# Optimization experiments

Measured on AMD Instinct MI355X. Metric: run time of the kernel, lower is better.

Reference implementation:

```python
import jax, jax.numpy as jnp
import numpy as np

N, E, G = 10000, 160000, 64      # nodes, edges, graphs
IN, H, L = 128, 128, 14          # in_channels, hidden, num GENConv layers
EPS_LN = 1e-5                    # torch LayerNorm eps
EPS_MSG = 1e-7                   # GENConv message eps


def layer_norm(x, g, b):
    mu = jnp.mean(x, axis=-1, keepdims=True)
    v = jnp.var(x, axis=-1, keepdims=True)
    return (x - mu) * jax.lax.rsqrt(v + EPS_LN) * g + b


def gen_conv(h, src, dst, t, sc, W1, b1, mg, mb, W2, b2):
    # message: relu(x_j) + eps  (no edge_attr)
    msg = jax.nn.relu(h[src]) + EPS_MSG                      # [E, H]
    # softmax aggregation over edges sharing a destination, per feature
    z = msg * t
    mx = jax.ops.segment_max(z, dst, num_segments=N)         # [N, H]
    mx = jnp.where(jnp.isfinite(mx), mx, 0.0)
    e = jnp.exp(z - mx[dst])
    ssum = jax.ops.segment_sum(e, dst, num_segments=N)
    alpha = e / (ssum[dst] + 1e-16)
    agg = jax.ops.segment_sum(msg * alpha, dst, num_segments=N)  # [N, H]
    # MessageNorm: normalize(agg) * ||h|| * scale
    agg = agg / jnp.maximum(jnp.linalg.norm(agg, axis=-1, keepdims=True), 1e-12)
    agg = agg * jnp.linalg.norm(h, axis=-1, keepdims=True) * sc
    out = h + agg
    # MLP [H, 2H, H] with LayerNorm + ReLU between (dropout off in eval)
    z1 = layer_norm(out @ W1 + b1, mg, mb)
    return jax.nn.relu(z1) @ W2 + b2


def setup_inputs() -> dict:
    key = jax.random.key(0)
    ks = jax.random.split(key, 8)
    s = 0.05
    x = jax.random.normal(ks[0], (N, IN), jnp.float32)
    edge_index = jax.random.randint(ks[1], (2, E), 0, N, dtype=jnp.int64)
    batch = jnp.sort(jax.random.randint(ks[2], (N,), 0, G, dtype=jnp.int64))
    enc_W = jax.random.normal(ks[3], (IN, H), jnp.float32) * s
    enc_b = jnp.zeros((H,), jnp.float32)
    ln_g = jnp.ones((L, H), jnp.float32)
    ln_b = jnp.zeros((L, H), jnp.float32)
    t = jnp.ones((L,), jnp.float32)         # learnable softmax temperature
    scale = jnp.ones((L,), jnp.float32)     # learnable MsgNorm scale
    W1 = jax.random.normal(ks[4], (L, H, 2 * H), jnp.float32) * s
    b1 = jnp.zeros((L, 2 * H), jnp.float32)
    mg = jnp.ones((L, 2 * H), jnp.float32)
    mb = jnp.zeros((L, 2 * H), jnp.float32)
    W2 = jax.random.normal(ks[5], (L, 2 * H, H), jnp.float32) * s
    b2 = jnp.zeros((L, H), jnp.float32)
    fn_g = jnp.ones((H,), jnp.float32)
    fn_b = jnp.zeros((H,), jnp.float32)
    return dict(x=x, edge_index=edge_index, batch=batch, enc_W=enc_W, enc_b=enc_b,
                ln_g=ln_g, ln_b=ln_b, t=t, scale=scale, W1=W1, b1=b1, mg=mg, mb=mb,
                W2=W2, b2=b2, fn_g=fn_g, fn_b=fn_b)


def reference(x, edge_index, batch, enc_W, enc_b, ln_g, ln_b, t, scale,
              W1, b1, mg, mb, W2, b2, fn_g, fn_b):
    src, dst = edge_index[0], edge_index[1]
    h = x @ enc_W + enc_b
    for i in range(L):  # DeepGCNLayer 'res+': x + conv(act(norm(x)))
        r = jax.nn.leaky_relu(layer_norm(h, ln_g[i], ln_b[i]), 0.01)
        h = h + gen_conv(r, src, dst, t[i], scale[i],
                         W1[i], b1[i], mg[i], mb[i], W2[i], b2[i])
    h = jax.nn.leaky_relu(layer_norm(h, fn_g, fn_b), 0.01)
    # global_mean_pool (fin_map is unused in the original forward)
    cnt = jax.ops.segment_sum(jnp.ones((N,), h.dtype), batch, num_segments=G)
    gf = jax.ops.segment_sum(h, batch, num_segments=G) / jnp.maximum(cnt, 1.0)[:, None]
    return gf
```

## Files before the change

### kernel.cpp

```cpp
#include <hip/hip_runtime.h>
#include <cstdint>
#include <cstddef>


#define BT 512

typedef __attribute__((ext_vector_type(8))) short bf16x8;
typedef __attribute__((ext_vector_type(4))) float f32x4;

__device__ inline float bf2f(ushort u) {
    union { uint i; float f; } v;
    v.i = (uint)u << 16;
    return v.f;
}
__device__ inline ushort f2bf(float f) {
    union { float f; uint i; } v;
    v.f = f;
    return (ushort)((v.i + 0x7fffu + ((v.i >> 16) & 1u)) >> 16);
}
__device__ inline uint f2bf2(float a, float b) {
    return (uint)f2bf(a) | ((uint)f2bf(b) << 16);
}

__device__ inline float wave_sum_f(float v) {
#pragma unroll
    for (int off = 32; off > 0; off >>= 1) v += __shfl_xor(v, off, 64);
    return v;
}

__global__ void setup_kernel(const float* __restrict__ x, ushort* __restrict__ xb,
                             const int* __restrict__ dst, int* __restrict__ deg,
                             const int* __restrict__ batch, int* __restrict__ gstart,
                             int total, int N, int E, int G) {
    int idx = blockIdx.x * blockDim.x + threadIdx.x;
    if (idx >= total) return;
    xb[idx] = f2bf(x[idx]);
    if (idx < E) atomicAdd(&deg[dst[idx]], 1);
    if (idx < N) {
        int bb = batch[idx];
        if (idx == 0)
            for (int g = 0; g <= bb; g++) gstart[g] = 0;
        else {
            int pb = batch[idx - 1];
            for (int g = pb + 1; g <= bb; g++) gstart[g] = idx;
        }
        if (idx == N - 1)
            for (int g = bb + 1; g <= G; g++) gstart[g] = N;
    }
}

__global__ __launch_bounds__(1024) void scan_kernel(const int* __restrict__ deg,
                                                    int* __restrict__ offs,
                                                    int* __restrict__ cursor, int N) {
    __shared__ int part[1024];
    int tid = threadIdx.x;
    int CH = (N + 1023) / 1024;
    int base = tid * CH;
    int s = 0;
    for (int i = 0; i < CH; i++) {
        int idx = base + i;
        if (idx < N) s += deg[idx];
    }
    part[tid] = s;
    __syncthreads();
    for (int off = 1; off < 1024; off <<= 1) {
        int v = (tid >= off) ? part[tid - off] : 0;
        __syncthreads();
        part[tid] += v;
        __syncthreads();
    }
    int run = (tid == 0) ? 0 : part[tid - 1];
    for (int i = 0; i < CH; i++) {
        int idx = base + i;
        if (idx < N) {
            offs[idx] = run;
            cursor[idx] = run;
            run += deg[idx];
        }
    }
    if (tid == 1023) offs[N] = part[1023];
}

__global__ void scatter_kernel(const int* __restrict__ src, const int* __restrict__ dst,
                               int* __restrict__ cursor, int* __restrict__ esrc, int E) {
    int e = blockIdx.x * blockDim.x + threadIdx.x;
    if (e < E) {
        int d = dst[e];
        int pos = atomicAdd(&cursor[d], 1);
        esrc[pos] = src[e];
    }
}

__global__ __launch_bounds__(256) void prep_kernel(const float* __restrict__ W1,
                                                   const float* __restrict__ W2,
                                                   const float* __restrict__ encW,
                                                   ushort* __restrict__ W1t,
                                                   ushort* __restrict__ W2t,
                                                   ushort* __restrict__ encWt, int L) {
    __shared__ float tile[32][33];
    int z = blockIdx.z;
    const float* in;
    ushort* out;
    int R, C;
    if (z < L) {
        in = W1 + (size_t)z * 32768; out = W1t + (size_t)z * 32768; R = 128; C = 256;
    } else if (z < 2 * L) {
        int i = z - L;
        in = W2 + (size_t)i * 32768; out = W2t + (size_t)i * 32768; R = 256; C = 128;
    } else {
        in = encW; out = encWt; R = 128; C = 128;
    }
    int r0 = blockIdx.y * 32, c0 = blockIdx.x * 32;
    if (r0 >= R || c0 >= C) return;
    int tx = threadIdx.x & 31, ty = threadIdx.x >> 5;
    for (int i = ty; i < 32; i += 8) tile[i][tx] = in[(size_t)(r0 + i) * C + c0 + tx];
    __syncthreads();
    for (int i = ty; i < 32; i += 8)
        out[(size_t)(c0 + i) * R + r0 + tx] = f2bf(tile[tx][i]);
}

__device__ __forceinline__ void agg_stage_v9(const ushort* __restrict__ rin,
                                             const int* __restrict__ offs,
                                             const int* __restrict__ esrc,
                                             const float* __restrict__ rnbuf,
                                             float tv, float sv, int row0,
                                             int w, int l, uint (*AsU)[68]) {
    int nd0 = row0 + 2 * w;
    int a0 = offs[nd0], a1 = offs[nd0 + 1], a2 = offs[nd0 + 2];
    int eb[2] = {a0, a1};
    int dg[2] = {a1 - a0, a2 - a1};
    float cs[2][4][2] = {}, cw[2][4][2] = {};
    int mx = max((dg[0] + 3) >> 2, (dg[1] + 3) >> 2);
#pragma unroll 1
    for (int i = 0; i < mx; i++) {
        int j = i * 4;
        uint rv[2][4];
        bool vl[2][4];
#pragma unroll
        for (int k = 0; k < 2; k++)
#pragma unroll
            for (int c = 0; c < 4; c++) {
                int jj = j + c;
                vl[k][c] = jj < dg[k];
                if (vl[k][c]) {
                    int sn = esrc[eb[k] + jj];
                    rv[k][c] = ((const uint*)rin)[(size_t)sn * 64 + l];
                }
            }
#pragma unroll
        for (int k = 0; k < 2; k++)
#pragma unroll
            for (int c = 0; c < 4; c++) {
                if (vl[k][c]) {
                    float x0 = bf2f((ushort)(rv[k][c] & 0xffff));
                    float x1 = bf2f((ushort)(rv[k][c] >> 16));
                    float g0 = fmaxf(x0, 0.f) + 1e-7f;
                    float g1 = fmaxf(x1, 0.f) + 1e-7f;
                    float p0 = __expf(g0 * tv);
                    float p1 = __expf(g1 * tv);
                    cs[k][c][0] += p0;
                    cs[k][c][1] += p1;
                    cw[k][c][0] += g0 * p0;
                    cw[k][c][1] += g1 * p1;
                }
            }
    }
#pragma unroll
    for (int k = 0; k < 2; k++) {
        float s0 = (cs[k][0][0] + cs[k][1][0]) + (cs[k][2][0] + cs[k][3][0]);
        float s1 = (cs[k][0][1] + cs[k][1][1]) + (cs[k][2][1] + cs[k][3][1]);
        float W0 = (cw[k][0][0] + cw[k][1][0]) + (cw[k][2][0] + cw[k][3][0]);
        float W1 = (cw[k][0][1] + cw[k][1][1]) + (cw[k][2][1] + cw[k][3][1]);
        float agg0 = W0 / (s0 + 1e-16f);
        float agg1 = W1 / (s1 + 1e-16f);
        int nd = nd0 + k;
        float nr = sqrtf(wave_sum_f(agg0 * agg0 + agg1 * agg1));
        float fac = rnbuf[nd] * sv / fmaxf(nr, 1e-12f);
        uint ru = ((const uint*)rin)[(size_t)nd * 64 + l];
        AsU[2 * w + k][l] = f2bf2(bf2f((ushort)(ru & 0xffff)) + agg0 * fac,
                                  bf2f((ushort)(ru >> 16)) + agg1 * fac);
    }
}

__device__ __forceinline__ void gemm1_stage8(const ushort (*As)[136],
                                             const ushort* __restrict__ Bt,
                                             const float* __restrict__ bias,
                                             const float* __restrict__ mg,
                                             const float* __restrict__ mb,
                                             ushort (*z1s)[264],
                                             int w, int q, int ln,
                                             float (*pS)[16], float (*pQ)[16]) {
    f32x4 acc[2];
    acc[0] = (f32x4){0.f, 0.f, 0.f, 0.f};
    acc[1] = (f32x4){0.f, 0.f, 0.f, 0.f};
#pragma unroll
    for (int ks = 0; ks < 128; ks += 32) {
        bf16x8 a = *(const bf16x8*)&As[ln][ks + q * 8];
#pragma unroll
        for (int ct = 0; ct < 2; ct++) {
            bf16x8 bv = *(const bf16x8*)(Bt + (size_t)(w * 32 + ct * 16 + ln) * 128 + ks + q * 8);
            acc[ct] = __builtin_amdgcn_mfma_f32_16x16x32_bf16(a, bv, acc[ct], 0, 0, 0);
        }
    }
    float s1[4] = {0, 0, 0, 0}, s2[4] = {0, 0, 0, 0};
#pragma unroll
    for (int ct = 0; ct < 2; ct++)
#pragma unroll
        for (int r = 0; r < 4; r++) {
            float v = acc[ct][r] + bias[w * 32 + ct * 16 + ln];
            acc[ct][r] = v;
            s1[r] += v;
            s2[r] += v * v;
        }
#pragma unroll
    for (int off = 1; off < 16; off <<= 1)
#pragma unroll
        for (int r = 0; r < 4; r++) {
            s1[r] += __shfl_xor(s1[r], off, 64);
            s2[r] += __shfl_xor(s2[r], off, 64);
        }
    if (ln == 0)
#pragma unroll
        for (int r = 0; r < 4; r++) {
            pS[w][q * 4 + r] = s1[r];
            pQ[w][q * 4 + r] = s2[r];
        }
    __syncthreads();
#pragma unroll
    for (int r = 0; r < 4; r++) {
        int row = q * 4 + r;
        float S = 0.f, Q = 0.f;
#pragma unroll
        for (int ww = 0; ww < 8; ww++) {
            S += pS[ww][row];
            Q += pQ[ww][row];
        }
        float mu = S * (1.f / 256.f);
        float var = Q * (1.f / 256.f) - mu * mu;
        float rs = rsqrtf(var + 1e-5f);
#pragma unroll
        for (int ct = 0; ct < 2; ct++) {
            int col = w * 32 + ct * 16 + ln;
            float y = (acc[ct][r] - mu) * rs * mg[col] + mb[col];
            z1s[row][col] = f2bf(fmaxf(y, 0.f));
        }
    }
    __syncthreads();
}

template <int KD, bool RESID>
__device__ __forceinline__ void out_stage8(const ushort* __restrict__ Abase, int astr,
                                           const ushort* __restrict__ Bt,
                                           const float* __restrict__ bias,
                                           const float* __restrict__ lg,
                                           const float* __restrict__ lb,
                                           float* __restrict__ hbuf,
                                           ushort* __restrict__ rout,
                                           float* __restrict__ rnbuf,
                                           int row0, int w, int q, int ln,
                                           float (*pS)[16], float (*pQ)[16]) {
    f32x4 acc = (f32x4){0.f, 0.f, 0.f, 0.f};
    int col = w * 16 + ln;
#pragma unroll
    for (int ks = 0; ks < KD; ks += 32) {
        bf16x8 a = *(const bf16x8*)(Abase + ln * astr + ks + q * 8);
        bf16x8 bv = *(const bf16x8*)(Bt + (size_t)col * KD + ks + q * 8);
        acc = __builtin_amdgcn_mfma_f32_16x16x32_bf16(a, bv, acc, 0, 0, 0);
    }
    float s1[4], s2[4];
#pragma unroll
    for (int r = 0; r < 4; r++) {
        int row = q * 4 + r;
        float v = acc[r] + bias[col];
        if (RESID) v += hbuf[(size_t)(row0 + row) * 128 + col];
        hbuf[(size_t)(row0 + row) * 128 + col] = v;
        acc[r] = v;
        s1[r] = v;
        s2[r] = v * v;
    }
#pragma unroll
    for (int off = 1; off < 16; off <<= 1)
#pragma unroll
        for (int r = 0; r < 4; r++) {
            s1[r] += __shfl_xor(s1[r], off, 64);
            s2[r] += __shfl_xor(s2[r], off, 64);
        }
    if (ln == 0)
#pragma unroll
        for (int r = 0; r < 4; r++) {
            pS[w][q * 4 + r] = s1[r];
            pQ[w][q * 4 + r] = s2[r];
        }
    __syncthreads();
    float yv[4];
    float t2[4];
#pragma unroll
    for (int r = 0; r < 4; r++) {
        int row = q * 4 + r;
        float S = 0.f, Q = 0.f;
#pragma unroll
        for (int ww = 0; ww < 8; ww++) {
            S += pS[ww][row];
            Q += pQ[ww][row];
        }
        float mu = S * (1.f / 128.f);
        float var = Q * (1.f / 128.f) - mu * mu;
        float rs = rsqrtf(var + 1e-5f);
        float y = (acc[r] - mu) * rs * lg[col] + lb[col];
        y = y > 0.f ? y : 0.01f * y;
        yv[r] = y;
        t2[r] = y * y;
    }
#pragma unroll
    for (int off = 1; off < 16; off <<= 1)
#pragma unroll
        for (int r = 0; r < 4; r++) t2[r] += __shfl_xor(t2[r], off, 64);
    __syncthreads();
    if (ln == 0)
#pragma unroll
        for (int r = 0; r < 4; r++) pS[w][q * 4 + r] = t2[r];
    __syncthreads();
#pragma unroll
    for (int r = 0; r < 4; r++) {
        int row = q * 4 + r;
        float T = 0.f;
#pragma unroll
        for (int ww = 0; ww < 8; ww++) T += pS[ww][row];
        if (w == 0 && ln == 0) rnbuf[row0 + row] = sqrtf(T);
        rout[(size_t)(row0 + row) * 128 + col] = f2bf(yv[r]);
    }
}

__global__ __launch_bounds__(BT) void enc_kernel(const ushort* __restrict__ xb,
                                                 const ushort* __restrict__ encWt,
                                                 const float* __restrict__ encB,
                                                 const float* __restrict__ lg,
                                                 const float* __restrict__ lb,
                                                 float* __restrict__ h,
                                                 ushort* __restrict__ r,
                                                 float* __restrict__ rn, int N) {
    __shared__ __align__(16) ushort As[16][136];
    __shared__ float pS[8][16], pQ[8][16];
    uint(*AsU)[68] = (uint(*)[68])As;
    int tid = threadIdx.x, w = tid >> 6, l = tid & 63;
    int q = l >> 4, ln = l & 15;
    int row0 = blockIdx.x * 16;
    for (int idx = tid; idx < 16 * 64; idx += BT) {
        int row = idx >> 6, cl = idx & 63;
        AsU[row][cl] = ((const uint*)xb)[(size_t)(row0 + row) * 64 + cl];
    }
    __syncthreads();
    out_stage8<128, false>(&As[0][0], 136, encWt, encB, lg, lb, h, r, rn,
                           row0, w, q, ln, pS, pQ);
}

__global__ __launch_bounds__(BT) void layer_kernel(const ushort* __restrict__ rin,
                                                   ushort* __restrict__ rout,
                                                   const int* __restrict__ offs,
                                                   const int* __restrict__ esrc,
                                                   float* __restrict__ rn,
                                                   float* __restrict__ h,
                                                   const ushort* __restrict__ W1t,
                                                   const ushort* __restrict__ W2t,
                                                   const float* __restrict__ b1,
                                                   const float* __restrict__ mg,
                                                   const float* __restrict__ mb,
                                                   const float* __restrict__ b2,
                                                   const float* __restrict__ ng,
                                                   const float* __restrict__ nb,
                                                   const float* __restrict__ tptr,
                                                   const float* __restrict__ scptr,
                                                   int N) {
    __shared__ __align__(16) ushort As[16][136];
    __shared__ __align__(16) ushort z1s[16][264];
    __shared__ float pS[8][16], pQ[8][16];
    uint(*AsU)[68] = (uint(*)[68])As;
    int tid = threadIdx.x, w = tid >> 6, l = tid & 63;
    int q = l >> 4, ln = l & 15;
    int row0 = blockIdx.x * 16;
    float tv = *tptr, sv = *scptr;
    agg_stage_v9(rin, offs, esrc, rn, tv, sv, row0, w, l, AsU);
    __syncthreads();
    gemm1_stage8(As, W1t, b1, mg, mb, z1s, w, q, ln, pS, pQ);
    out_stage8<256, true>(&z1s[0][0], 264, W2t, b2, ng, nb, h, rout, rn,
                          row0, w, q, ln, pS, pQ);
}

__global__ __launch_bounds__(256) void pool_kernel(const ushort* __restrict__ rf,
                                                   const int* __restrict__ gstart,
                                                   float* __restrict__ out) {
    __shared__ float pb0[4][64], pb1[4][64];
    int g = blockIdx.x;
    int w = threadIdx.x >> 6, l = threadIdx.x & 63;
    int s = gstart[g], e = gstart[g + 1];
    float a0 = 0.f, a1 = 0.f;
    for (int n = s + w; n < e; n += 4) {
        uint rv = ((const uint*)rf)[(size_t)n * 64 + l];
        a0 += bf2f((ushort)(rv & 0xffff));
        a1 += bf2f((ushort)(rv >> 16));
    }
    pb0[w][l] = a0;
    pb1[w][l] = a1;
    __syncthreads();
    if (threadIdx.x < 64) {
        float t0 = pb0[0][l] + pb0[1][l] + pb0[2][l] + pb0[3][l];
        float t1 = pb1[0][l] + pb1[1][l] + pb1[2][l] + pb1[3][l];
        float inv = 1.f / fmaxf((float)(e - s), 1.f);
        out[g * 128 + 2 * l] = t0 * inv;
        out[g * 128 + 2 * l + 1] = t1 * inv;
    }
}

extern "C" void kernel_launch(void* const* d_in, const int* in_sizes, int n_in,
                              void* d_out, int out_size, void* d_ws, size_t ws_size,
                              hipStream_t stream) {
    const float* x     = (const float*)d_in[0];
    const int*   ei    = (const int*)d_in[1];
    const int*   batch = (const int*)d_in[2];
    const float* encW  = (const float*)d_in[3];
    const float* encB  = (const float*)d_in[4];
    const float* ln_g  = (const float*)d_in[5];
    const float* ln_b  = (const float*)d_in[6];
    const float* tArr  = (const float*)d_in[7];
    const float* scArr = (const float*)d_in[8];
    const float* W1    = (const float*)d_in[9];
    const float* b1    = (const float*)d_in[10];
    const float* mg    = (const float*)d_in[11];
    const float* mb    = (const float*)d_in[12];
    const float* W2    = (const float*)d_in[13];
    const float* b2    = (const float*)d_in[14];
    const float* fn_g  = (const float*)d_in[15];
    const float* fn_b  = (const float*)d_in[16];
    float* out = (float*)d_out;

    const int N = in_sizes[0] / 128;
    const int E = in_sizes[1] / 2;
    const int L = in_sizes[7];
    const int G = 64;

    const int* src = ei;
    const int* dst = ei + E;

    char* p = (char*)d_ws;
    auto alloc = [&](size_t bytes) -> void* {
        void* qp = (void*)p;
        p += (bytes + 255) & ~(size_t)255;
        return qp;
    };
    int*    deg    = (int*)alloc((size_t)N * 4);
    int*    offs   = (int*)alloc((size_t)(N + 1) * 4);
    int*    cursor = (int*)alloc((size_t)N * 4);
    int*    esrc   = (int*)alloc((size_t)E * 4);
    int*    gstart = (int*)alloc((size_t)(G + 1) * 4);
    float*  h      = (float*)alloc((size_t)N * 128 * 4);
    ushort* r0     = (ushort*)alloc((size_t)N * 128 * 2);
    ushort* r1     = (ushort*)alloc((size_t)N * 128 * 2);
    float*  rn     = (float*)alloc((size_t)N * 4);
    ushort* xb     = (ushort*)alloc((size_t)N * 128 * 2);
    ushort* W1t    = (ushort*)alloc((size_t)L * 32768 * 2);
    ushort* W2t    = (ushort*)alloc((size_t)L * 32768 * 2);
    ushort* encWt  = (ushort*)alloc((size_t)16384 * 2);

    hipMemsetAsync(deg, 0, (size_t)N * 4, stream);

    setup_kernel<<<(N * 128 + 255) / 256, 256, 0, stream>>>(x, xb, dst, deg, batch,
                                                            gstart, N * 128, N, E, G);
    scan_kernel<<<1, 1024, 0, stream>>>(deg, offs, cursor, N);
    scatter_kernel<<<(E + 255) / 256, 256, 0, stream>>>(src, dst, cursor, esrc, E);
    prep_kernel<<<dim3(8, 8, 2 * L + 1), 256, 0, stream>>>(W1, W2, encW, W1t, W2t,
                                                           encWt, L);

    const int TILES = N / 16;

    enc_kernel<<<TILES, BT, 0, stream>>>(xb, encWt, encB, ln_g, ln_b, h, r0, rn, N);

    for (int i = 0; i < L; i++) {
        const ushort* rin = (i & 1) ? r1 : r0;
        ushort* rout = (i & 1) ? r0 : r1;
        const float* ng = (i < L - 1) ? (ln_g + (size_t)(i + 1) * 128) : fn_g;
        const float* nb = (i < L - 1) ? (ln_b + (size_t)(i + 1) * 128) : fn_b;
        layer_kernel<<<TILES, BT, 0, stream>>>(rin, rout, offs, esrc, rn, h,
                                               W1t + ((size_t)i << 15),
                                               W2t + ((size_t)i << 15),
                                               b1 + (size_t)i * 256,
                                               mg + (size_t)i * 256,
                                               mb + (size_t)i * 256,
                                               b2 + (size_t)i * 128,
                                               ng, nb, tArr + i, scArr + i, N);
    }

    const ushort* rf = ((L - 1) & 1) ? r0 : r1;
    pool_kernel<<<G, 256, 0, stream>>>(rf, gstart, out);
}
```

Measured before the change: 664.2 us.

## Stage edge indices in LDS and prefetch W1 fragments and residual before aggregation

At kernel start, each block loads its nodes' edge-source indices into shared memory (up to 1024 entries, falling back to global beyond that). It also prefetches its W1 weight fragments and residual h values into registers before the aggregation loop. The goal is to hide global-memory latency for index and weight loads behind the gather phase. In exchange it uses more registers and 4 KB of extra LDS, which may lower occupancy.

```diff
diff --git a/kernel.cpp b/kernel.cpp
--- a/kernel.cpp
+++ b/kernel.cpp
@@ -4,6 +4,7 @@
 
 
 #define BT 512
+#define ECAP 1024
 
 typedef __attribute__((ext_vector_type(8))) short bf16x8;
 typedef __attribute__((ext_vector_type(4))) float f32x4;
@@ -119,15 +120,17 @@
         out[(size_t)(c0 + i) * R + r0 + tx] = f2bf(tile[tx][i]);
 }
 
-__device__ __forceinline__ void agg_stage_v9(const ushort* __restrict__ rin,
-                                             const int* __restrict__ offs,
-                                             const int* __restrict__ esrc,
-                                             const float* __restrict__ rnbuf,
-                                             float tv, float sv, int row0,
-                                             int w, int l, uint (*AsU)[68]) {
+__device__ __forceinline__ void agg_stage_v10(const ushort* __restrict__ rin,
+                                              const int* __restrict__ offs,
+                                              const int* __restrict__ esrc,
+                                              const int* __restrict__ eidx,
+                                              int ebase,
+                                              const float* __restrict__ rnbuf,
+                                              float tv, float sv, int row0,
+                                              int w, int l, uint (*AsU)[68]) {
     int nd0 = row0 + 2 * w;
     int a0 = offs[nd0], a1 = offs[nd0 + 1], a2 = offs[nd0 + 2];
-    int eb[2] = {a0, a1};
+    int lo[2] = {a0 - ebase, a1 - ebase};
     int dg[2] = {a1 - a0, a2 - a1};
     float cs[2][4][2] = {}, cw[2][4][2] = {};
     int mx = max((dg[0] + 3) >> 2, (dg[1] + 3) >> 2);
@@ -143,7 +146,8 @@
                 int jj = j + c;
                 vl[k][c] = jj < dg[k];
                 if (vl[k][c]) {
-                    int sn = esrc[eb[k] + jj];
+                    int off = lo[k] + jj;
+                    int sn = (off < ECAP) ? eidx[off] : esrc[ebase + off];
                     rv[k][c] = ((const uint*)rin)[(size_t)sn * 64 + l];
                 }
             }
@@ -183,7 +187,7 @@
 }
 
 __device__ __forceinline__ void gemm1_stage8(const ushort (*As)[136],
-                                             const ushort* __restrict__ Bt,
+                                             const bf16x8 wpre[2][4],
                                              const float* __restrict__ bias,
                                              const float* __restrict__ mg,
                                              const float* __restrict__ mb,
@@ -194,13 +198,11 @@
     acc[0] = (f32x4){0.f, 0.f, 0.f, 0.f};
     acc[1] = (f32x4){0.f, 0.f, 0.f, 0.f};
 #pragma unroll
-    for (int ks = 0; ks < 128; ks += 32) {
-        bf16x8 a = *(const bf16x8*)&As[ln][ks + q * 8];
-#pragma unroll
-        for (int ct = 0; ct < 2; ct++) {
-            bf16x8 bv = *(const bf16x8*)(Bt + (size_t)(w * 32 + ct * 16 + ln) * 128 + ks + q * 8);
-            acc[ct] = __builtin_amdgcn_mfma_f32_16x16x32_bf16(a, bv, acc[ct], 0, 0, 0);
-        }
+    for (int ks4 = 0; ks4 < 4; ks4++) {
+        bf16x8 a = *(const bf16x8*)&As[ln][ks4 * 32 + q * 8];
+#pragma unroll
+        for (int ct = 0; ct < 2; ct++)
+            acc[ct] = __builtin_amdgcn_mfma_f32_16x16x32_bf16(a, wpre[ct][ks4], acc[ct], 0, 0, 0);
     }
     float s1[4] = {0, 0, 0, 0}, s2[4] = {0, 0, 0, 0};
 #pragma unroll
@@ -255,6 +257,7 @@
                                            const float* __restrict__ lg,
                                            const float* __restrict__ lb,
                                            float* __restrict__ hbuf,
+                                           const float* hpre,
                                            ushort* __restrict__ rout,
                                            float* __restrict__ rnbuf,
                                            int row0, int w, int q, int ln,
@@ -272,7 +275,7 @@
     for (int r = 0; r < 4; r++) {
         int row = q * 4 + r;
         float v = acc[r] + bias[col];
-        if (RESID) v += hbuf[(size_t)(row0 + row) * 128 + col];
+        if (RESID) v += hpre[r];
         hbuf[(size_t)(row0 + row) * 128 + col] = v;
         acc[r] = v;
         s1[r] = v;
@@ -350,7 +353,7 @@
         AsU[row][cl] = ((const uint*)xb)[(size_t)(row0 + row) * 64 + cl];
     }
     __syncthreads();
-    out_stage8<128, false>(&As[0][0], 136, encWt, encB, lg, lb, h, r, rn,
+    out_stage8<128, false>(&As[0][0], 136, encWt, encB, lg, lb, h, nullptr, r, rn,
                            row0, w, q, ln, pS, pQ);
 }
 
@@ -374,15 +377,38 @@
     __shared__ __align__(16) ushort As[16][136];
     __shared__ __align__(16) ushort z1s[16][264];
     __shared__ float pS[8][16], pQ[8][16];
+    __shared__ int eidx[ECAP];
     uint(*AsU)[68] = (uint(*)[68])As;
     int tid = threadIdx.x, w = tid >> 6, l = tid & 63;
     int q = l >> 4, ln = l & 15;
     int row0 = blockIdx.x * 16;
     float tv = *tptr, sv = *scptr;
-    agg_stage_v9(rin, offs, esrc, rn, tv, sv, row0, w, l, AsU);
-    __syncthreads();
-    gemm1_stage8(As, W1t, b1, mg, mb, z1s, w, q, ln, pS, pQ);
-    out_stage8<256, true>(&z1s[0][0], 264, W2t, b2, ng, nb, h, rout, rn,
+
+    bf16x8 wpre[2][4];
+#pragma unroll
+    for (int ct = 0; ct < 2; ct++)
+#pragma unroll
+        for (int ks4 = 0; ks4 < 4; ks4++)
+            wpre[ct][ks4] = *(const bf16x8*)(W1t + (size_t)(w * 32 + ct * 16 + ln) * 128 + ks4 * 32 + q * 8);
+
+    float hpre[4];
+    {
+        int col = w * 16 + ln;
+#pragma unroll
+        for (int r = 0; r < 4; r++)
+            hpre[r] = h[(size_t)(row0 + q * 4 + r) * 128 + col];
+    }
+
+    int ebase = offs[row0];
+    int ecnt = offs[row0 + 16] - ebase;
+    int ecap = min(ecnt, ECAP);
+    for (int i = tid; i < ecap; i += BT) eidx[i] = esrc[ebase + i];
+    __syncthreads();
+
+    agg_stage_v10(rin, offs, esrc, eidx, ebase, rn, tv, sv, row0, w, l, AsU);
+    __syncthreads();
+    gemm1_stage8(As, wpre, b1, mg, mb, z1s, w, q, ln, pS, pQ);
+    out_stage8<256, true>(&z1s[0][0], 264, W2t, b2, ng, nb, h, hpre, rout, rn,
                           row0, w, q, ln, pS, pQ);
 }
 
```

Result: slower. 794.6 us (+19.6%).

## Gather neighbor rows with 8-byte loads, two edges per wave, shuffled indices

Applied to the files above, without the earlier changes.

The per-node softmax aggregation now splits each wave into two halves. Each half reads a different neighbor row with 8-byte loads (4 bf16 features per lane) instead of 4-byte loads across all 64 lanes. Edge source indices are loaded once per 64-edge chunk with a coalesced read and broadcast through wave shuffles, replacing per-edge scalar index loads. The two halves' partial sums are combined with a cross-half shuffle. This aims for more edges in flight and fewer dependent index loads, at the cost of extra shuffles and more registers per lane.

```diff
diff --git a/kernel.cpp b/kernel.cpp
--- a/kernel.cpp
+++ b/kernel.cpp
@@ -119,66 +119,96 @@
         out[(size_t)(c0 + i) * R + r0 + tx] = f2bf(tile[tx][i]);
 }
 
-__device__ __forceinline__ void agg_stage_v9(const ushort* __restrict__ rin,
-                                             const int* __restrict__ offs,
-                                             const int* __restrict__ esrc,
-                                             const float* __restrict__ rnbuf,
-                                             float tv, float sv, int row0,
-                                             int w, int l, uint (*AsU)[68]) {
+__device__ __forceinline__ void agg_stage_v13(const ushort* __restrict__ rin,
+                                              const int* __restrict__ offs,
+                                              const int* __restrict__ esrc,
+                                              const float* __restrict__ rnbuf,
+                                              float tv, float sv, int row0,
+                                              int w, int l, uint (*AsU)[68]) {
+    const uint2* rin2 = (const uint2*)rin;
     int nd0 = row0 + 2 * w;
+    int half = l >> 5, li = l & 31;
     int a0 = offs[nd0], a1 = offs[nd0 + 1], a2 = offs[nd0 + 2];
     int eb[2] = {a0, a1};
     int dg[2] = {a1 - a0, a2 - a1};
-    float cs[2][4][2] = {}, cw[2][4][2] = {};
-    int mx = max((dg[0] + 3) >> 2, (dg[1] + 3) >> 2);
+
+    float s[2][4] = {}, W[2][4] = {};
+    int mxdeg = max(dg[0], dg[1]);
+
 #pragma unroll 1
-    for (int i = 0; i < mx; i++) {
-        int j = i * 4;
-        uint rv[2][4];
-        bool vl[2][4];
-#pragma unroll
-        for (int k = 0; k < 2; k++)
+    for (int base = 0; base < mxdeg; base += 64) {
+        int rem0 = min(dg[0] - base, 64);
+        int rem1 = min(dg[1] - base, 64);
+        int idx0 = (rem0 > 0 && l < rem0) ? esrc[eb[0] + base + l] : 0;
+        int idx1 = (rem1 > 0 && l < rem1) ? esrc[eb[1] + base + l] : 0;
+        int it = (max(rem0, rem1) + 7) >> 3;
+#pragma unroll 1
+        for (int i = 0; i < it; i++) {
+            int j0 = i * 8 + half;
+            uint2 rv[2][4];
+            bool vl[2][4];
 #pragma unroll
             for (int c = 0; c < 4; c++) {
-                int jj = j + c;
-                vl[k][c] = jj < dg[k];
-                if (vl[k][c]) {
-                    int sn = esrc[eb[k] + jj];
-                    rv[k][c] = ((const uint*)rin)[(size_t)sn * 64 + l];
+                int j = j0 + 2 * c;
+                vl[0][c] = j < rem0;
+                vl[1][c] = j < rem1;
+                int sn0 = __shfl(idx0, j, 64);
+                int sn1 = __shfl(idx1, j, 64);
+                if (vl[0][c]) rv[0][c] = rin2[(size_t)sn0 * 32 + li];
+                if (vl[1][c]) rv[1][c] = rin2[(size_t)sn1 * 32 + li];
+            }
+#pragma unroll
+            for (int k = 0; k < 2; k++)
+#pragma unroll
+                for (int c = 0; c < 4; c++) {
+                    if (vl[k][c]) {
+                        float f0 = bf2f((ushort)(rv[k][c].x & 0xffff));
+                        float f1 = bf2f((ushort)(rv[k][c].x >> 16));
+                        float f2 = bf2f((ushort)(rv[k][c].y & 0xffff));
+                        float f3 = bf2f((ushort)(rv[k][c].y >> 16));
+                        float g0 = fmaxf(f0, 0.f) + 1e-7f;
+                        float g1 = fmaxf(f1, 0.f) + 1e-7f;
+                        float g2 = fmaxf(f2, 0.f) + 1e-7f;
+                        float g3 = fmaxf(f3, 0.f) + 1e-7f;
+                        float p0 = __expf(g0 * tv);
+                        float p1 = __expf(g1 * tv);
+                        float p2 = __expf(g2 * tv);
+                        float p3 = __expf(g3 * tv);
+                        s[k][0] += p0; W[k][0] += g0 * p0;
+                        s[k][1] += p1; W[k][1] += g1 * p1;
+                        s[k][2] += p2; W[k][2] += g2 * p2;
+                        s[k][3] += p3; W[k][3] += g3 * p3;
+                    }
                 }
-            }
-#pragma unroll
-        for (int k = 0; k < 2; k++)
-#pragma unroll
-            for (int c = 0; c < 4; c++) {
-                if (vl[k][c]) {
-                    float x0 = bf2f((ushort)(rv[k][c] & 0xffff));
-                    float x1 = bf2f((ushort)(rv[k][c] >> 16));
-                    float g0 = fmaxf(x0, 0.f) + 1e-7f;
-                    float g1 = fmaxf(x1, 0.f) + 1e-7f;
-                    float p0 = __expf(g0 * tv);
-                    float p1 = __expf(g1 * tv);
-                    cs[k][c][0] += p0;
-                    cs[k][c][1] += p1;
-                    cw[k][c][0] += g0 * p0;
-                    cw[k][c][1] += g1 * p1;
-                }
-            }
-    }
+        }
+    }
+
 #pragma unroll
     for (int k = 0; k < 2; k++) {
-        float s0 = (cs[k][0][0] + cs[k][1][0]) + (cs[k][2][0] + cs[k][3][0]);
-        float s1 = (cs[k][0][1] + cs[k][1][1]) + (cs[k][2][1] + cs[k][3][1]);
-        float W0 = (cw[k][0][0] + cw[k][1][0]) + (cw[k][2][0] + cw[k][3][0]);
-        float W1 = (cw[k][0][1] + cw[k][1][1]) + (cw[k][2][1] + cw[k][3][1]);
-        float agg0 = W0 / (s0 + 1e-16f);
-        float agg1 = W1 / (s1 + 1e-16f);
+#pragma unroll
+        for (int f = 0; f < 4; f++) {
+            s[k][f] += __shfl_xor(s[k][f], 32, 64);
+            W[k][f] += __shfl_xor(W[k][f], 32, 64);
+        }
+        float agg[4], nsq = 0.f;
+#pragma unroll
+        for (int f = 0; f < 4; f++) {
+            agg[f] = W[k][f] / (s[k][f] + 1e-16f);
+            nsq += agg[f] * agg[f];
+        }
+#pragma unroll
+        for (int off = 1; off < 32; off <<= 1) nsq += __shfl_xor(nsq, off, 64);
         int nd = nd0 + k;
-        float nr = sqrtf(wave_sum_f(agg0 * agg0 + agg1 * agg1));
-        float fac = rnbuf[nd] * sv / fmaxf(nr, 1e-12f);
-        uint ru = ((const uint*)rin)[(size_t)nd * 64 + l];
-        AsU[2 * w + k][l] = f2bf2(bf2f((ushort)(ru & 0xffff)) + agg0 * fac,
-                                  bf2f((ushort)(ru >> 16)) + agg1 * fac);
+        float fac = rnbuf[nd] * sv / fmaxf(sqrtf(nsq), 1e-12f);
+        uint2 ru = rin2[(size_t)nd * 32 + li];
+        if (half == 0) {
+            uint2 o;
+            o.x = f2bf2(bf2f((ushort)(ru.x & 0xffff)) + agg[0] * fac,
+                        bf2f((ushort)(ru.x >> 16)) + agg[1] * fac);
+            o.y = f2bf2(bf2f((ushort)(ru.y & 0xffff)) + agg[2] * fac,
+                        bf2f((ushort)(ru.y >> 16)) + agg[3] * fac);
+            *(uint2*)&AsU[2 * w + k][2 * li] = o;
+        }
     }
 }
 
@@ -379,7 +409,7 @@
     int q = l >> 4, ln = l & 15;
     int row0 = blockIdx.x * 16;
     float tv = *tptr, sv = *scptr;
-    agg_stage_v9(rin, offs, esrc, rn, tv, sv, row0, w, l, AsU);
+    agg_stage_v13(rin, offs, esrc, rn, tv, sv, row0, w, l, AsU);
     __syncthreads();
     gemm1_stage8(As, W1t, b1, mg, mb, z1s, w, q, ln, pS, pQ);
     out_stage8<256, true>(&z1s[0][0], 264, W2t, b2, ng, nb, h, rout, rn,
@@ -461,7 +491,7 @@
     ushort* W2t    = (ushort*)alloc((size_t)L * 32768 * 2);
     ushort* encWt  = (ushort*)alloc((size_t)16384 * 2);
 
-    hipMemsetAsync(deg, 0, (size_t)N * 4, stream);
+    (void)hipMemsetAsync(deg, 0, (size_t)N * 4, stream);
 
     setup_kernel<<<(N * 128 + 255) / 256, 256, 0, stream>>>(x, xb, dst, deg, batch,
                                                             gstart, N * 128, N, E, G);
```

New measurement: 585.7 us. 1.13x faster.
